# Kernel optimization log

Measured on AMD Instinct MI355X. Metric: run time of the kernel, lower is better.

Reference implementation:

```python
import jax, jax.numpy as jnp
import numpy as np

H, W = 512, 512          # pseudo_image_dims
C = 32                   # feat_channels == MHA embed_dim
NH, HD = 2, 16           # heads, head_dim
B, NL, NR = 2, 50000, 20000
EPS = 1e-5
SCALE = np.float32(1.0 / np.sqrt(HD))

# 3x3 neighbor shifts used by shift_bev_grids (INDEX_SHIFT in source)
INDEX_SHIFT = jnp.array([[0, 0], [-1, 0], [1, 0], [0, 1], [-1, 1], [1, 1], [0, -1], [-1, -1], [1, -1]], dtype=jnp.int32)
# 5x5 shifts used by new_gen_dy_coor (gen_index_shift(2))
SHIFT25 = jnp.array([[i, j] for i in range(-2, 3) for j in range(-2, 3)], dtype=jnp.int32)


def _unique_coords(key, n):
    perm = jax.random.permutation(key, H * W)[:n]
    return jnp.stack([perm // W, perm % W], axis=1).astype(jnp.int32)


def setup_inputs():
    key = jax.random.key(0)
    ks = jax.random.split(key, 8)
    inp = {
        "li_bev_feats": jax.random.normal(ks[0], (B, NL, C), jnp.float32),
        "li_bev_coors": jnp.stack([_unique_coords(jax.random.fold_in(ks[1], b), NL) for b in range(B)]),
        "ra_bev_feats": jax.random.normal(ks[2], (B, NR, C), jnp.float32),
        "ra_bev_coors": jnp.stack([_unique_coords(jax.random.fold_in(ks[3], b), NR) for b in range(B)]),
        "radar_bev_dy": jax.random.bernoulli(ks[4], 0.3, (B, NR)),
    }
    pk = jax.random.split(ks[5], 12)
    w = lambda k, o, i: 0.05 * jax.random.normal(k, (o, i), jnp.float32)
    z = lambda n: jnp.zeros((n,), jnp.float32)
    inp.update(
        ln_li_w=jnp.ones((C,), jnp.float32), ln_li_b=z(C),
        ln_ra_w=jnp.ones((C,), jnp.float32), ln_ra_b=z(C),
        q1_w=w(pk[0], C, C), q1_b=z(C), k1_w=w(pk[1], C, C), k1_b=z(C), v1_w=w(pk[2], C, C), v1_b=z(C),
        q2_w=w(pk[3], C, C), q2_b=z(C), k2_w=w(pk[4], C, C), k2_b=z(C), v2_w=w(pk[5], C, C), v2_b=z(C),
        pos_w=w(pk[6], C, 2), pos_b=z(C),
        a1_in_w=w(pk[7], 3 * C, C), a1_in_b=z(3 * C), a1_out_w=w(pk[8], C, C), a1_out_b=z(C),
        a2_in_w=w(pk[9], 3 * C, C), a2_in_b=z(3 * C), a2_out_w=w(pk[10], C, C), a2_out_b=z(C),
    )
    return inp


def _ln(x, w, b):
    mu = jnp.mean(x, -1, keepdims=True)
    var = jnp.mean(jnp.square(x - mu), -1, keepdims=True)
    return (x - mu) / jnp.sqrt(var + EPS) * w + b


def _grid_of(coors, n):
    # dense coord -> pillar-index lookup table, -1 for empty cells
    return jnp.full((H, W), -1, jnp.int32).at[coors[:, 0], coors[:, 1]].set(jnp.arange(n, dtype=jnp.int32))


def _gather_kv(coors, grid, k_map, v_map, pe9):
    # per pillar: look up the 3x3 shifted neighbors in the OTHER modality's grid
    sh = coors[:, None, :] + INDEX_SHIFT[None]                      # [N,9,2]
    inb = (sh[..., 0] >= 0) & (sh[..., 0] < H) & (sh[..., 1] >= 0) & (sh[..., 1] < W)
    idx = grid[jnp.clip(sh[..., 0], 0, H - 1), jnp.clip(sh[..., 1], 0, W - 1)]
    valid = (inb & (idx >= 0))[..., None]                           # [N,9,1]
    safe = jnp.clip(idx, 0, None)
    k = jnp.where(valid, k_map[safe], 0.0)                          # masked_fill(~cond, 0)
    v = jnp.where(valid, v_map[safe] + pe9[None], 0.0)              # pos-enc added before masking
    return k, v


def _mha(q, k, v, Wi, bi, Wo, bo):
    # torch MultiheadAttention (batch_first, eval -> no dropout); q [N,1,C], k/v [N,9,C]
    n = q.shape[0]
    qp = (q @ Wi[:C].T + bi[:C]).reshape(n, 1, NH, HD)
    kp = (k @ Wi[C:2 * C].T + bi[C:2 * C]).reshape(n, -1, NH, HD)
    vp = (v @ Wi[2 * C:].T + bi[2 * C:]).reshape(n, -1, NH, HD)
    s = jnp.einsum("nqhd,nkhd->nhqk", qp, kp) * SCALE
    a = jax.nn.softmax(s, axis=-1)
    o = jnp.einsum("nhqk,nkhd->nqhd", a, vp).reshape(n, C)
    return o @ Wo.T + bo


def _scatter(coors, feat):
    # PointPillarsScatter: place [N,C] features at their (x,y) cells of a [C,H,W] canvas
    return jnp.zeros((H, W, C), feat.dtype).at[coors[:, 0], coors[:, 1]].set(feat).transpose(2, 0, 1)


def _forward(li_bev_feats, li_bev_coors, ra_bev_feats, ra_bev_coors, radar_bev_dy,
             ln_li_w, ln_li_b, ln_ra_w, ln_ra_b,
             q1_w, q1_b, k1_w, k1_b, v1_w, v1_b,
             q2_w, q2_b, k2_w, k2_b, v2_w, v2_b,
             pos_w, pos_b,
             a1_in_w, a1_in_b, a1_out_w, a1_out_b,
             a2_in_w, a2_in_b, a2_out_w, a2_out_b):
    pe9 = INDEX_SHIFT.astype(jnp.float32) @ pos_w.T + pos_b        # [9,C] positional codes

    def per_sample(li_f, li_c, ra_f, ra_c, ra_dy):
        li_n = _ln(li_f, ln_li_w, ln_li_b)
        ra_n = _ln(ra_f, ln_ra_w, ln_ra_b)
        li_grid = _grid_of(li_c, NL)
        ra_grid = _grid_of(ra_c, NR)
        # new_gen_dy_coor: lidar pillars within a 5x5 (mod dims+1) window of any dynamic radar pillar
        g = jnp.array([H + 1, W + 1], jnp.int32)
        sh = (ra_c[:, None, :] + SHIFT25[None]) % g                # [NR,25,2]
        inb = (sh[..., 0] < H) & (sh[..., 1] < W)
        idx = li_grid[jnp.clip(sh[..., 0], 0, H - 1), jnp.clip(sh[..., 1], 0, W - 1)]
        valid = inb & (idx >= 0) & ra_dy[:, None]
        dy_mask = jnp.zeros(NL + 1, bool).at[jnp.where(valid, idx, NL).reshape(-1)].set(True)[:NL]
        # branch 1: dynamic lidar queries cross-attend to 3x3 radar neighbors
        q1 = li_n @ q1_w.T + q1_b
        k1 = ra_n @ k1_w.T + k1_b
        v1 = ra_n @ v1_w.T + v1_b
        k, v = _gather_kv(li_c, ra_grid, k1, v1, pe9)
        out1 = _mha(q1[:, None, :], k, v, a1_in_w, a1_in_b, a1_out_w, a1_out_b)
        out1 = out1 * dy_mask[:, None].astype(out1.dtype)          # only dy pillars scattered
        img_li = _scatter(li_c, out1)
        # branch 2: radar queries cross-attend to 3x3 lidar neighbors
        q2 = ra_n @ q2_w.T + q2_b
        k2 = li_n @ k2_w.T + k2_b
        v2 = li_n @ v2_w.T + v2_b
        k, v = _gather_kv(ra_c, li_grid, k2, v2, pe9)
        out2 = _mha(q2[:, None, :], k, v, a2_in_w, a2_in_b, a2_out_w, a2_out_b)
        img_ra = _scatter(ra_c, out2)
        return img_li, img_ra

    return jax.vmap(per_sample)(li_bev_feats, li_bev_coors, ra_bev_feats, ra_bev_coors, radar_bev_dy)


def reference(li_bev_feats, li_bev_coors, ra_bev_feats, ra_bev_coors, radar_bev_dy,
              ln_li_w, ln_li_b, ln_ra_w, ln_ra_b,
              q1_w, q1_b, k1_w, k1_b, v1_w, v1_b,
              q2_w, q2_b, k2_w, k2_b, v2_w, v2_b,
              pos_w, pos_b,
              a1_in_w, a1_in_b, a1_out_w, a1_out_b,
              a2_in_w, a2_in_b, a2_out_w, a2_out_b):
    return _forward(li_bev_feats, li_bev_coors, ra_bev_feats, ra_bev_coors, radar_bev_dy,
                    ln_li_w, ln_li_b, ln_ra_w, ln_ra_b,
                    q1_w, q1_b, k1_w, k1_b, v1_w, v1_b,
                    q2_w, q2_b, k2_w, k2_b, v2_w, v2_b,
                    pos_w, pos_b,
                    a1_in_w, a1_in_b, a1_out_w, a1_out_b,
                    a2_in_w, a2_in_b, a2_out_w, a2_out_b)
```

## Files before the change

### kernel.cpp

```cpp
#include <hip/hip_runtime.h>
#include <stdint.h>

constexpr int Hh = 512, Ww = 512;
constexpr int HW = Hh * Ww;
constexpr int C  = 32;
constexpr int B  = 2;
constexpr int NL = 50000;
constexpr int NR = 20000;
constexpr float EPS = 1e-5f;
constexpr float SCALE = 0.25f;

constexpr int GBL = (NL + NR + 255) / 256;
constexpr int LB  = (NL + 255) / 256;
constexpr int RB  = (NR + 255) / 256;
constexpr int NTILE = 1024;

__device__ __constant__ int DX9[9] = {0,-1,1,0,-1,1,0,-1,1};
__device__ __constant__ int DY9[9] = {0,0,0,1,1,1,-1,-1,-1};

__device__ __forceinline__ int xcd_swz(int bid, int nb) {
    int q = nb >> 3, r = nb & 7;
    int xcd = bid & 7, idx = bid >> 3;
    return (xcd < r) ? xcd * (q + 1) + idx : r * (q + 1) + (xcd - r) * q + idx;
}

__global__ void count_k(const int* __restrict__ li_c, const int* __restrict__ ra_c,
                        int* __restrict__ cnt) {
    int b = blockIdx.y;
    int i = blockIdx.x * 256 + threadIdx.x;
    if (i < NL) {
        int x = li_c[((size_t)b * NL + i) * 2 + 0];
        int y = li_c[((size_t)b * NL + i) * 2 + 1];
        int tile = ((x >> 4) << 5) | (y >> 4);
        atomicAdd(&cnt[(b * 2 + 0) * NTILE + tile], 1);
    } else if (i < NL + NR) {
        int j = i - NL;
        int x = ra_c[((size_t)b * NR + j) * 2 + 0];
        int y = ra_c[((size_t)b * NR + j) * 2 + 1];
        int tile = ((x >> 4) << 5) | (y >> 4);
        atomicAdd(&cnt[(b * 2 + 1) * NTILE + tile], 1);
    }
}

__global__ void scan_k(const int* __restrict__ cnt, int* __restrict__ cursor) {
    int g = blockIdx.x;
    const int* c = cnt + g * NTILE;
    int* cur = cursor + g * NTILE;
    __shared__ int s[NTILE];
    int t = threadIdx.x;
    int self = c[t];
    s[t] = self;
    __syncthreads();
    for (int off = 1; off < NTILE; off <<= 1) {
        int v = (t >= off) ? s[t - off] : 0;
        __syncthreads();
        s[t] += v;
        __syncthreads();
    }
    cur[t] = s[t] - self;
}

__global__ void scatter_proj_k(const int* __restrict__ li_c, const int* __restrict__ ra_c,
                               const int* __restrict__ ra_dy,
                               int* __restrict__ li_grid, int* __restrict__ ra_grid,
                               uint8_t* __restrict__ rdy_grid, int* __restrict__ cursor,
                               int* __restrict__ lixy, int* __restrict__ raxy,
                               const float* __restrict__ li_f, const float* __restrict__ ra_f,
                               const float* __restrict__ ln_li_w, const float* __restrict__ ln_li_b,
                               const float* __restrict__ ln_ra_w, const float* __restrict__ ln_ra_b,
                               const float* __restrict__ a1iw, const float* __restrict__ a1ib,
                               const float* __restrict__ a2iw, const float* __restrict__ a2ib,
                               const float* __restrict__ q1w, const float* __restrict__ q1b,
                               const float* __restrict__ k1w, const float* __restrict__ k1b,
                               const float* __restrict__ v1w, const float* __restrict__ v1b,
                               const float* __restrict__ q2w, const float* __restrict__ q2b,
                               const float* __restrict__ k2w, const float* __restrict__ k2b,
                               const float* __restrict__ v2w, const float* __restrict__ v2b,
                               float* __restrict__ qp1, float* __restrict__ kp1, float* __restrict__ vp1,
                               float* __restrict__ qp2, float* __restrict__ kp2, float* __restrict__ vp2) {
    int bx = blockIdx.x, b = blockIdx.y, t = threadIdx.x;
    bool lidar = (bx < LB);
    int n = lidar ? NL : NR;
    int i = (lidar ? bx : bx - LB) * 256 + t;

    const float* feats = lidar ? li_f : ra_f;
    const float* lnw = lidar ? ln_li_w : ln_ra_w;
    const float* lnb = lidar ? ln_li_b : ln_ra_b;
    const float* Asec[3] = { (lidar ? a1iw : a2iw) + 0 * C * C,
                             (lidar ? a2iw : a1iw) + 1 * C * C,
                             (lidar ? a2iw : a1iw) + 2 * C * C };
    const float* absec[3] = { (lidar ? a1ib : a2ib) + 0 * C,
                              (lidar ? a2ib : a1ib) + 1 * C,
                              (lidar ? a2ib : a1ib) + 2 * C };
    const float* Wsec[3] = { lidar ? q1w : q2w, lidar ? k2w : k1w, lidar ? v2w : v1w };
    const float* bsec[3] = { lidar ? q1b : q2b, lidar ? k2b : k1b, lidar ? v2b : v1b };
    float* outp[3] = { lidar ? qp1 : qp2, lidar ? kp2 : kp1, lidar ? vp2 : vp1 };

    __shared__ float sM[3][1024];
    __shared__ float sc[3][32];
    for (int p = t; p < 3072; p += 256) {
        int m = p >> 10, e = p & 1023, r = e >> 5, d = e & 31;
        float s = 0.f;
        #pragma unroll
        for (int c = 0; c < C; ++c) s += Asec[m][r * C + c] * Wsec[m][c * C + d];
        sM[m][e] = s;
    }
    if (t < 96) {
        int m = t >> 5, r = t & 31;
        float s = absec[m][r];
        #pragma unroll
        for (int c = 0; c < C; ++c) s += Asec[m][r * C + c] * bsec[m][c];
        sc[m][r] = s;
    }
    __syncthreads();
    if (i >= n) return;

    int x = (lidar ? li_c : ra_c)[((size_t)b * n + i) * 2 + 0];
    int y = (lidar ? li_c : ra_c)[((size_t)b * n + i) * 2 + 1];
    int tile = ((x >> 4) << 5) | (y >> 4);
    int mod = lidar ? 0 : 1;
    int slot = atomicAdd(&cursor[(b * 2 + mod) * NTILE + tile], 1);
    size_t cellg = (size_t)b * HW + x * Ww + y;
    if (lidar) {
        li_grid[cellg] = slot;
        lixy[(size_t)b * NL + slot] = (x << 16) | y;
    } else {
        ra_grid[cellg] = slot;
        raxy[(size_t)b * NR + slot] = (x << 16) | y;
        if (ra_dy[(size_t)b * n + i] != 0) rdy_grid[cellg] = 0;
    }

    float xv[C];
    const float4* f4 = (const float4*)(feats + ((size_t)b * n + i) * C);
    #pragma unroll
    for (int q = 0; q < 8; ++q) {
        float4 tv = f4[q];
        xv[4*q] = tv.x; xv[4*q+1] = tv.y; xv[4*q+2] = tv.z; xv[4*q+3] = tv.w;
    }
    float mu = 0.f;
    #pragma unroll
    for (int c = 0; c < C; ++c) mu += xv[c];
    mu *= (1.0f / C);
    float var = 0.f;
    #pragma unroll
    for (int c = 0; c < C; ++c) { float d = xv[c] - mu; var += d * d; }
    var *= (1.0f / C);
    float inv = 1.0f / sqrtf(var + EPS);
    #pragma unroll
    for (int c = 0; c < C; ++c) xv[c] = (xv[c] - mu) * inv * lnw[c] + lnb[c];

    #pragma unroll
    for (int m = 0; m < 3; ++m) {
        float4* o4 = (float4*)(outp[m] + ((size_t)b * n + slot) * C);
        #pragma unroll
        for (int rq = 0; rq < 8; ++rq) {
            float4 tv;
            float* tp = &tv.x;
            #pragma unroll
            for (int rr = 0; rr < 4; ++rr) {
                int r = rq * 4 + rr;
                float s = sc[m][r];
                #pragma unroll
                for (int d = 0; d < C; ++d) s += sM[m][r * C + d] * xv[d];
                tp[rr] = s;
            }
            o4[rq] = tv;
        }
    }
}

__device__ __forceinline__ void attn_cell(
        int x, int y,
        const float* __restrict__ qrow,
        const float* __restrict__ kmap, const float* __restrict__ vmap,
        const int* __restrict__ kv_grid,
        const float* sWo, const float* sbo, const float* spe,
        const float* skinv, const float* svinv,
        float* v) {
    int nidx[9];
    #pragma unroll
    for (int j = 0; j < 9; ++j) {
        int sx = x + DX9[j], sy = y + DY9[j];
        nidx[j] = (sx >= 0 && sx < Hh && sy >= 0 && sy < Ww) ? kv_grid[sx * Ww + sy] : -1;
    }
    float qp[C];
    const float4* qp4 = (const float4*)qrow;
    #pragma unroll
    for (int q = 0; q < 8; ++q) {
        float4 tv = qp4[q];
        qp[4*q] = tv.x; qp[4*q+1] = tv.y; qp[4*q+2] = tv.z; qp[4*q+3] = tv.w;
    }
    float sc0[9], sc1[9];
    #pragma unroll
    for (int j = 0; j < 9; ++j) {
        int idx = nidx[j];
        const float4* kp4 = (idx >= 0) ? (const float4*)(kmap + (size_t)idx * C)
                                       : (const float4*)skinv;
        float s0 = 0.f, s1 = 0.f;
        #pragma unroll
        for (int q = 0; q < 4; ++q) {
            float4 tv = kp4[q];
            s0 += qp[4*q] * tv.x + qp[4*q+1] * tv.y + qp[4*q+2] * tv.z + qp[4*q+3] * tv.w;
        }
        #pragma unroll
        for (int q = 4; q < 8; ++q) {
            float4 tv = kp4[q];
            s1 += qp[4*q] * tv.x + qp[4*q+1] * tv.y + qp[4*q+2] * tv.z + qp[4*q+3] * tv.w;
        }
        sc0[j] = s0 * SCALE; sc1[j] = s1 * SCALE;
    }
    float m0 = sc0[0], m1 = sc1[0];
    #pragma unroll
    for (int j = 1; j < 9; ++j) { m0 = fmaxf(m0, sc0[j]); m1 = fmaxf(m1, sc1[j]); }
    float sum0 = 0.f, sum1 = 0.f;
    #pragma unroll
    for (int j = 0; j < 9; ++j) {
        sc0[j] = expf(sc0[j] - m0); sum0 += sc0[j];
        sc1[j] = expf(sc1[j] - m1); sum1 += sc1[j];
    }
    float r0 = 1.0f / sum0, r1 = 1.0f / sum1;

    float o[C];
    #pragma unroll
    for (int c = 0; c < C; ++c) o[c] = 0.f;
    #pragma unroll
    for (int j = 0; j < 9; ++j) {
        float a0 = sc0[j] * r0, a1 = sc1[j] * r1;
        int idx = nidx[j];
        if (idx >= 0) {
            const float4* vp4 = (const float4*)(vmap + (size_t)idx * C);
            #pragma unroll
            for (int q = 0; q < 8; ++q) {
                float4 tv = vp4[q];
                float a = (q < 4) ? a0 : a1;
                o[4*q]   += a * (tv.x + spe[j * 32 + 4*q]);
                o[4*q+1] += a * (tv.y + spe[j * 32 + 4*q+1]);
                o[4*q+2] += a * (tv.z + spe[j * 32 + 4*q+2]);
                o[4*q+3] += a * (tv.w + spe[j * 32 + 4*q+3]);
            }
        } else {
            #pragma unroll
            for (int d = 0; d < 16; ++d) {
                o[d]      += a0 * svinv[d];
                o[16 + d] += a1 * svinv[16 + d];
            }
        }
    }
    #pragma unroll
    for (int r = 0; r < C; ++r) {
        float s = sbo[r];
        #pragma unroll
        for (int c = 0; c < C; ++c) s += sWo[r * C + c] * o[c];
        v[r] = s;
    }
}

__global__ void attn_slot_k(const int* __restrict__ li_grid, const int* __restrict__ ra_grid,
                            const uint8_t* __restrict__ rdy_grid,
                            const int* __restrict__ lixy, const int* __restrict__ raxy,
                            const float* __restrict__ qp1, const float* __restrict__ kp1,
                            const float* __restrict__ vp1, const float* __restrict__ qp2,
                            const float* __restrict__ kp2, const float* __restrict__ vp2,
                            const float* __restrict__ a1iw, const float* __restrict__ a1ib,
                            const float* __restrict__ a2iw, const float* __restrict__ a2ib,
                            const float* __restrict__ posw, const float* __restrict__ posb,
                            const float* __restrict__ a1ow, const float* __restrict__ a1ob,
                            const float* __restrict__ a2ow, const float* __restrict__ a2ob,
                            float* __restrict__ feat1, float* __restrict__ feat2) {
    int wg = xcd_swz(blockIdx.x, LB + RB);
    bool br1 = (wg < LB);
    int n = br1 ? NL : NR;
    int i = (br1 ? wg : wg - LB) * 256 + threadIdx.x;
    int b = blockIdx.y;
    int t = threadIdx.x;

    const float* Wo = br1 ? a1ow : a2ow;
    const float* bo = br1 ? a1ob : a2ob;
    const float* Aib = br1 ? a1ib : a2ib;
    const float* Av  = (br1 ? a1iw : a2iw) + 2 * C * C;
    __shared__ alignas(16) float sWo[1024];
    __shared__ alignas(16) float sbo[32], skinv[32], svinv[32];
    __shared__ alignas(16) float spe[288];
    for (int p = t; p < 1024; p += 256) sWo[p] = Wo[p];
    if (t < 32) {
        sbo[t] = bo[t];
        skinv[t] = Aib[32 + t];
        svinv[t] = Aib[64 + t];
    }
    for (int e = t; e < 288; e += 256) {
        int j = e >> 5, r = e & 31;
        float sx = (float)DX9[j], sy = (float)DY9[j];
        float s = 0.f;
        #pragma unroll
        for (int c = 0; c < C; ++c) {
            float pe = posw[c * 2 + 0] * sx + posw[c * 2 + 1] * sy + posb[c];
            s += Av[r * C + c] * pe;
        }
        spe[e] = s;
    }
    __syncthreads();
    if (i >= n) return;

    int pc = (br1 ? lixy : raxy)[(size_t)b * n + i];
    int x = pc >> 16, y = pc & 0xFFFF;

    float v[C];
    if (br1) {
        const uint8_t* rdy = rdy_grid + (size_t)b * HW;
        bool dy = false;
        #pragma unroll
        for (int dx = -2; dx <= 2 && !dy; ++dx) {
            int cx = x + dx;
            cx = (cx < 0) ? cx + 513 : (cx >= 513 ? cx - 513 : cx);
            if (cx == 512) continue;
            #pragma unroll
            for (int dyy = -2; dyy <= 2; ++dyy) {
                int cy = y + dyy;
                cy = (cy < 0) ? cy + 513 : (cy >= 513 ? cy - 513 : cy);
                if (cy == 512) continue;
                if (rdy[cx * Ww + cy] == 0) { dy = true; break; }
            }
        }
        if (dy) {
            attn_cell(x, y, qp1 + ((size_t)b * NL + i) * C,
                      kp1 + (size_t)b * NR * C, vp1 + (size_t)b * NR * C,
                      ra_grid + (size_t)b * HW, sWo, sbo, spe, skinv, svinv, v);
        } else {
            #pragma unroll
            for (int c = 0; c < C; ++c) v[c] = 0.f;
        }
        float4* o4 = (float4*)(feat1 + ((size_t)b * NL + i) * C);
        #pragma unroll
        for (int q = 0; q < 8; ++q) o4[q] = *(float4*)&v[4*q];
    } else {
        attn_cell(x, y, qp2 + ((size_t)b * NR + i) * C,
                  kp2 + (size_t)b * NL * C, vp2 + (size_t)b * NL * C,
                  li_grid + (size_t)b * HW, sWo, sbo, spe, skinv, svinv, v);
        float4* o4 = (float4*)(feat2 + ((size_t)b * NR + i) * C);
        #pragma unroll
        for (int q = 0; q < 8; ++q) o4[q] = *(float4*)&v[4*q];
    }
}

__global__ void canvas_k(const int* __restrict__ li_grid, const int* __restrict__ ra_grid,
                         const float* __restrict__ feat1, const float* __restrict__ feat2,
                         float* __restrict__ out_li, float* __restrict__ out_ra) {
    int b = blockIdx.y;
    int wg = xcd_swz(blockIdx.x, HW / 256);
    int cell = wg * 256 + threadIdx.x;
    size_t gidx = (size_t)b * HW + cell;
    size_t obase = (size_t)b * C * HW + cell;

    int li = li_grid[gidx];
    float v[C];
    if (li >= 0) {
        const float4* f = (const float4*)(feat1 + ((size_t)b * NL + li) * C);
        #pragma unroll
        for (int q = 0; q < 8; ++q) {
            float4 t = f[q];
            v[4*q] = t.x; v[4*q+1] = t.y; v[4*q+2] = t.z; v[4*q+3] = t.w;
        }
    } else {
        #pragma unroll
        for (int c = 0; c < C; ++c) v[c] = 0.f;
    }
    #pragma unroll
    for (int c = 0; c < C; ++c) out_li[obase + (size_t)c * HW] = v[c];

    int ra = ra_grid[gidx];
    if (ra >= 0) {
        const float4* f = (const float4*)(feat2 + ((size_t)b * NR + ra) * C);
        #pragma unroll
        for (int q = 0; q < 8; ++q) {
            float4 t = f[q];
            v[4*q] = t.x; v[4*q+1] = t.y; v[4*q+2] = t.z; v[4*q+3] = t.w;
        }
    } else {
        #pragma unroll
        for (int c = 0; c < C; ++c) v[c] = 0.f;
    }
    #pragma unroll
    for (int c = 0; c < C; ++c) out_ra[obase + (size_t)c * HW] = v[c];
}

extern "C" void kernel_launch(void* const* d_in, const int* in_sizes, int n_in,
                              void* d_out, int out_size, void* d_ws, size_t ws_size,
                              hipStream_t stream) {
    const float*   li_f  = (const float*)d_in[0];
    const int*     li_c  = (const int*)d_in[1];
    const float*   ra_f  = (const float*)d_in[2];
    const int*     ra_c  = (const int*)d_in[3];
    const int*     ra_dy = (const int*)d_in[4];
    const float* ln_li_w = (const float*)d_in[5];
    const float* ln_li_b = (const float*)d_in[6];
    const float* ln_ra_w = (const float*)d_in[7];
    const float* ln_ra_b = (const float*)d_in[8];
    const float* q1w = (const float*)d_in[9],  *q1b = (const float*)d_in[10];
    const float* k1w = (const float*)d_in[11], *k1b = (const float*)d_in[12];
    const float* v1w = (const float*)d_in[13], *v1b = (const float*)d_in[14];
    const float* q2w = (const float*)d_in[15], *q2b = (const float*)d_in[16];
    const float* k2w = (const float*)d_in[17], *k2b = (const float*)d_in[18];
    const float* v2w = (const float*)d_in[19], *v2b = (const float*)d_in[20];
    const float* posw = (const float*)d_in[21], *posb = (const float*)d_in[22];
    const float* a1iw = (const float*)d_in[23], *a1ib = (const float*)d_in[24];
    const float* a1ow = (const float*)d_in[25], *a1ob = (const float*)d_in[26];
    const float* a2iw = (const float*)d_in[27], *a2ib = (const float*)d_in[28];
    const float* a2ow = (const float*)d_in[29], *a2ob = (const float*)d_in[30];

    char* ws = (char*)d_ws;
    size_t off = 0;
    auto carve = [&](size_t bytes) { void* p = ws + off; off += (bytes + 255) & ~(size_t)255; return p; };
    int*     li_grid  = (int*)carve((size_t)B * HW * 4);
    int*     ra_grid  = (int*)carve((size_t)B * HW * 4);
    uint8_t* rdy_grid = (uint8_t*)carve((size_t)B * HW);
    size_t   init_bytes = off;
    int*     cnt      = (int*)carve((size_t)4 * NTILE * 4);
    int*     cursor   = (int*)carve((size_t)4 * NTILE * 4);
    int*     lixy     = (int*)carve((size_t)B * NL * 4);
    int*     raxy     = (int*)carve((size_t)B * NR * 4);
    float*   qp1 = (float*)carve((size_t)B * NL * C * 4);
    float*   kp1 = (float*)carve((size_t)B * NR * C * 4);
    float*   vp1 = (float*)carve((size_t)B * NR * C * 4);
    float*   qp2 = (float*)carve((size_t)B * NR * C * 4);
    float*   kp2 = (float*)carve((size_t)B * NL * C * 4);
    float*   vp2 = (float*)carve((size_t)B * NL * C * 4);
    float*   feat1 = (float*)carve((size_t)B * NL * C * 4);
    float*   feat2 = (float*)carve((size_t)B * NR * C * 4);
    (void)ws_size; (void)n_in; (void)in_sizes; (void)out_size;

    float* out_li = (float*)d_out;
    float* out_ra = out_li + (size_t)B * C * HW;

    hipMemsetAsync(li_grid, 0xFF, init_bytes, stream);
    hipMemsetAsync(cnt, 0, (size_t)4 * NTILE * 4, stream);

    count_k<<<dim3(GBL, B), dim3(256), 0, stream>>>(li_c, ra_c, cnt);
    scan_k<<<dim3(4), dim3(NTILE), 0, stream>>>(cnt, cursor);
    scatter_proj_k<<<dim3(LB + RB, B), dim3(256), 0, stream>>>(
        li_c, ra_c, ra_dy, li_grid, ra_grid, rdy_grid, cursor, lixy, raxy,
        li_f, ra_f, ln_li_w, ln_li_b, ln_ra_w, ln_ra_b,
        a1iw, a1ib, a2iw, a2ib,
        q1w, q1b, k1w, k1b, v1w, v1b, q2w, q2b, k2w, k2b, v2w, v2b,
        qp1, kp1, vp1, qp2, kp2, vp2);
    attn_slot_k<<<dim3(LB + RB, B), dim3(256), 0, stream>>>(
        li_grid, ra_grid, rdy_grid, lixy, raxy,
        qp1, kp1, vp1, qp2, kp2, vp2,
        a1iw, a1ib, a2iw, a2ib, posw, posb, a1ow, a1ob, a2ow, a2ob,
        feat1, feat2);
    canvas_k<<<dim3(HW / 256, B), dim3(256), 0, stream>>>(
        li_grid, ra_grid, feat1, feat2, out_li, out_ra);
}
```

Before: 405.3 us.

## Split attention across two threads per query, one per head, and drop XCD swizzle

The attention kernel now assigns two threads to each query, one per head. Each thread computes its head's scores, softmax and weighted V sum, plus a partial output projection, and the partials are combined with a lane shuffle. This cuts per-thread register pressure and doubles the thread count, aiming for better occupancy and latency hiding on the gathers. The XCD block swizzle is also removed from the attention and canvas kernels, which may change L2 locality. The cost is duplicated neighbor-index lookups and dynamic-check work in both threads.

```diff
diff --git a/kernel.cpp b/kernel.cpp
--- a/kernel.cpp
+++ b/kernel.cpp
@@ -13,16 +13,12 @@
 constexpr int GBL = (NL + NR + 255) / 256;
 constexpr int LB  = (NL + 255) / 256;
 constexpr int RB  = (NR + 255) / 256;
+constexpr int LB2 = (NL + 127) / 128;
+constexpr int RB2 = (NR + 127) / 128;
 constexpr int NTILE = 1024;
 
 __device__ __constant__ int DX9[9] = {0,-1,1,0,-1,1,0,-1,1};
 __device__ __constant__ int DY9[9] = {0,0,0,1,1,1,-1,-1,-1};
-
-__device__ __forceinline__ int xcd_swz(int bid, int nb) {
-    int q = nb >> 3, r = nb & 7;
-    int xcd = bid & 7, idx = bid >> 3;
-    return (xcd < r) ? xcd * (q + 1) + idx : r * (q + 1) + (xcd - r) * q + idx;
-}
 
 __global__ void count_k(const int* __restrict__ li_c, const int* __restrict__ ra_c,
                         int* __restrict__ cnt) {
@@ -169,92 +165,6 @@
     }
 }
 
-__device__ __forceinline__ void attn_cell(
-        int x, int y,
-        const float* __restrict__ qrow,
-        const float* __restrict__ kmap, const float* __restrict__ vmap,
-        const int* __restrict__ kv_grid,
-        const float* sWo, const float* sbo, const float* spe,
-        const float* skinv, const float* svinv,
-        float* v) {
-    int nidx[9];
-    #pragma unroll
-    for (int j = 0; j < 9; ++j) {
-        int sx = x + DX9[j], sy = y + DY9[j];
-        nidx[j] = (sx >= 0 && sx < Hh && sy >= 0 && sy < Ww) ? kv_grid[sx * Ww + sy] : -1;
-    }
-    float qp[C];
-    const float4* qp4 = (const float4*)qrow;
-    #pragma unroll
-    for (int q = 0; q < 8; ++q) {
-        float4 tv = qp4[q];
-        qp[4*q] = tv.x; qp[4*q+1] = tv.y; qp[4*q+2] = tv.z; qp[4*q+3] = tv.w;
-    }
-    float sc0[9], sc1[9];
-    #pragma unroll
-    for (int j = 0; j < 9; ++j) {
-        int idx = nidx[j];
-        const float4* kp4 = (idx >= 0) ? (const float4*)(kmap + (size_t)idx * C)
-                                       : (const float4*)skinv;
-        float s0 = 0.f, s1 = 0.f;
-        #pragma unroll
-        for (int q = 0; q < 4; ++q) {
-            float4 tv = kp4[q];
-            s0 += qp[4*q] * tv.x + qp[4*q+1] * tv.y + qp[4*q+2] * tv.z + qp[4*q+3] * tv.w;
-        }
-        #pragma unroll
-        for (int q = 4; q < 8; ++q) {
-            float4 tv = kp4[q];
-            s1 += qp[4*q] * tv.x + qp[4*q+1] * tv.y + qp[4*q+2] * tv.z + qp[4*q+3] * tv.w;
-        }
-        sc0[j] = s0 * SCALE; sc1[j] = s1 * SCALE;
-    }
-    float m0 = sc0[0], m1 = sc1[0];
-    #pragma unroll
-    for (int j = 1; j < 9; ++j) { m0 = fmaxf(m0, sc0[j]); m1 = fmaxf(m1, sc1[j]); }
-    float sum0 = 0.f, sum1 = 0.f;
-    #pragma unroll
-    for (int j = 0; j < 9; ++j) {
-        sc0[j] = expf(sc0[j] - m0); sum0 += sc0[j];
-        sc1[j] = expf(sc1[j] - m1); sum1 += sc1[j];
-    }
-    float r0 = 1.0f / sum0, r1 = 1.0f / sum1;
-
-    float o[C];
-    #pragma unroll
-    for (int c = 0; c < C; ++c) o[c] = 0.f;
-    #pragma unroll
-    for (int j = 0; j < 9; ++j) {
-        float a0 = sc0[j] * r0, a1 = sc1[j] * r1;
-        int idx = nidx[j];
-        if (idx >= 0) {
-            const float4* vp4 = (const float4*)(vmap + (size_t)idx * C);
-            #pragma unroll
-            for (int q = 0; q < 8; ++q) {
-                float4 tv = vp4[q];
-                float a = (q < 4) ? a0 : a1;
-                o[4*q]   += a * (tv.x + spe[j * 32 + 4*q]);
-                o[4*q+1] += a * (tv.y + spe[j * 32 + 4*q+1]);
-                o[4*q+2] += a * (tv.z + spe[j * 32 + 4*q+2]);
-                o[4*q+3] += a * (tv.w + spe[j * 32 + 4*q+3]);
-            }
-        } else {
-            #pragma unroll
-            for (int d = 0; d < 16; ++d) {
-                o[d]      += a0 * svinv[d];
-                o[16 + d] += a1 * svinv[16 + d];
-            }
-        }
-    }
-    #pragma unroll
-    for (int r = 0; r < C; ++r) {
-        float s = sbo[r];
-        #pragma unroll
-        for (int c = 0; c < C; ++c) s += sWo[r * C + c] * o[c];
-        v[r] = s;
-    }
-}
-
 __global__ void attn_slot_k(const int* __restrict__ li_grid, const int* __restrict__ ra_grid,
                             const uint8_t* __restrict__ rdy_grid,
                             const int* __restrict__ lixy, const int* __restrict__ raxy,
@@ -267,12 +177,13 @@
                             const float* __restrict__ a1ow, const float* __restrict__ a1ob,
                             const float* __restrict__ a2ow, const float* __restrict__ a2ob,
                             float* __restrict__ feat1, float* __restrict__ feat2) {
-    int wg = xcd_swz(blockIdx.x, LB + RB);
-    bool br1 = (wg < LB);
+    int bx = blockIdx.x;
+    bool br1 = (bx < LB2);
     int n = br1 ? NL : NR;
-    int i = (br1 ? wg : wg - LB) * 256 + threadIdx.x;
+    int t = threadIdx.x;
+    int qi = (br1 ? bx : bx - LB2) * 128 + (t >> 1);
+    int h  = t & 1;
     int b = blockIdx.y;
-    int t = threadIdx.x;
 
     const float* Wo = br1 ? a1ow : a2ow;
     const float* bo = br1 ? a1ob : a2ob;
@@ -299,12 +210,12 @@
         spe[e] = s;
     }
     __syncthreads();
-    if (i >= n) return;
-
-    int pc = (br1 ? lixy : raxy)[(size_t)b * n + i];
+    if (qi >= n) return;
+
+    int pc = (br1 ? lixy : raxy)[(size_t)b * n + qi];
     int x = pc >> 16, y = pc & 0xFFFF;
-
-    float v[C];
+    float* featrow = (br1 ? feat1 : feat2) + ((size_t)b * n + qi) * C;
+
     if (br1) {
         const uint8_t* rdy = rdy_grid + (size_t)b * HW;
         bool dy = false;
@@ -321,24 +232,105 @@
                 if (rdy[cx * Ww + cy] == 0) { dy = true; break; }
             }
         }
-        if (dy) {
-            attn_cell(x, y, qp1 + ((size_t)b * NL + i) * C,
-                      kp1 + (size_t)b * NR * C, vp1 + (size_t)b * NR * C,
-                      ra_grid + (size_t)b * HW, sWo, sbo, spe, skinv, svinv, v);
+        if (!dy) {
+            if (h == 0) {
+                float4 z = {0.f, 0.f, 0.f, 0.f};
+                float4* o4 = (float4*)featrow;
+                #pragma unroll
+                for (int q = 0; q < 8; ++q) o4[q] = z;
+            }
+            return;
+        }
+    }
+
+    const int* kv_grid = (br1 ? ra_grid : li_grid) + (size_t)b * HW;
+    int nkv = br1 ? NR : NL;
+    const float* kmap = (br1 ? kp1 : kp2) + (size_t)b * nkv * C;
+    const float* vmap = (br1 ? vp1 : vp2) + (size_t)b * nkv * C;
+
+    int nidx[9];
+    #pragma unroll
+    for (int j = 0; j < 9; ++j) {
+        int sx = x + DX9[j], sy = y + DY9[j];
+        nidx[j] = (sx >= 0 && sx < Hh && sy >= 0 && sy < Ww) ? kv_grid[sx * Ww + sy] : -1;
+    }
+
+    float qh[16];
+    {
+        const float4* q4 = (const float4*)((br1 ? qp1 : qp2) + ((size_t)b * n + qi) * C + h * 16);
+        #pragma unroll
+        for (int q = 0; q < 4; ++q) {
+            float4 tv = q4[q];
+            qh[4*q] = tv.x; qh[4*q+1] = tv.y; qh[4*q+2] = tv.z; qh[4*q+3] = tv.w;
+        }
+    }
+
+    float sc[9];
+    #pragma unroll
+    for (int j = 0; j < 9; ++j) {
+        int idx = nidx[j];
+        const float4* kp4 = (idx >= 0) ? (const float4*)(kmap + (size_t)idx * C + h * 16)
+                                       : (const float4*)(skinv + h * 16);
+        float s = 0.f;
+        #pragma unroll
+        for (int q = 0; q < 4; ++q) {
+            float4 tv = kp4[q];
+            s += qh[4*q] * tv.x + qh[4*q+1] * tv.y + qh[4*q+2] * tv.z + qh[4*q+3] * tv.w;
+        }
+        sc[j] = s * SCALE;
+    }
+    float m0 = sc[0];
+    #pragma unroll
+    for (int j = 1; j < 9; ++j) m0 = fmaxf(m0, sc[j]);
+    float sum = 0.f;
+    #pragma unroll
+    for (int j = 0; j < 9; ++j) { sc[j] = expf(sc[j] - m0); sum += sc[j]; }
+    float rs = 1.0f / sum;
+
+    float o[16];
+    #pragma unroll
+    for (int d = 0; d < 16; ++d) o[d] = 0.f;
+    #pragma unroll
+    for (int j = 0; j < 9; ++j) {
+        float a = sc[j] * rs;
+        int idx = nidx[j];
+        if (idx >= 0) {
+            const float4* vp4 = (const float4*)(vmap + (size_t)idx * C + h * 16);
+            #pragma unroll
+            for (int q = 0; q < 4; ++q) {
+                float4 tv = vp4[q];
+                o[4*q]   += a * (tv.x + spe[j * 32 + h * 16 + 4*q]);
+                o[4*q+1] += a * (tv.y + spe[j * 32 + h * 16 + 4*q+1]);
+                o[4*q+2] += a * (tv.z + spe[j * 32 + h * 16 + 4*q+2]);
+                o[4*q+3] += a * (tv.w + spe[j * 32 + h * 16 + 4*q+3]);
+            }
         } else {
             #pragma unroll
-            for (int c = 0; c < C; ++c) v[c] = 0.f;
-        }
-        float4* o4 = (float4*)(feat1 + ((size_t)b * NL + i) * C);
-        #pragma unroll
-        for (int q = 0; q < 8; ++q) o4[q] = *(float4*)&v[4*q];
-    } else {
-        attn_cell(x, y, qp2 + ((size_t)b * NR + i) * C,
-                  kp2 + (size_t)b * NL * C, vp2 + (size_t)b * NL * C,
-                  li_grid + (size_t)b * HW, sWo, sbo, spe, skinv, svinv, v);
-        float4* o4 = (float4*)(feat2 + ((size_t)b * NR + i) * C);
-        #pragma unroll
-        for (int q = 0; q < 8; ++q) o4[q] = *(float4*)&v[4*q];
+            for (int d = 0; d < 16; ++d) o[d] += a * svinv[h * 16 + d];
+        }
+    }
+
+    float P[32];
+    #pragma unroll
+    for (int r = 0; r < C; ++r) {
+        float s = 0.f;
+        #pragma unroll
+        for (int c = 0; c < 16; ++c) s += sWo[r * C + h * 16 + c] * o[c];
+        P[r] = s;
+    }
+    #pragma unroll
+    for (int r = 0; r < C; ++r) P[r] += __shfl_xor(P[r], 1);
+    if (h == 0) {
+        float4* o4 = (float4*)featrow;
+        #pragma unroll
+        for (int rq = 0; rq < 8; ++rq) {
+            float4 tv;
+            tv.x = P[4*rq]   + sbo[4*rq];
+            tv.y = P[4*rq+1] + sbo[4*rq+1];
+            tv.z = P[4*rq+2] + sbo[4*rq+2];
+            tv.w = P[4*rq+3] + sbo[4*rq+3];
+            o4[rq] = tv;
+        }
     }
 }
 
@@ -346,8 +338,7 @@
                          const float* __restrict__ feat1, const float* __restrict__ feat2,
                          float* __restrict__ out_li, float* __restrict__ out_ra) {
     int b = blockIdx.y;
-    int wg = xcd_swz(blockIdx.x, HW / 256);
-    int cell = wg * 256 + threadIdx.x;
+    int cell = blockIdx.x * 256 + threadIdx.x;
     size_t gidx = (size_t)b * HW + cell;
     size_t obase = (size_t)b * C * HW + cell;
 
@@ -442,7 +433,7 @@
         a1iw, a1ib, a2iw, a2ib,
         q1w, q1b, k1w, k1b, v1w, v1b, q2w, q2b, k2w, k2b, v2w, v2b,
         qp1, kp1, vp1, qp2, kp2, vp2);
-    attn_slot_k<<<dim3(LB + RB, B), dim3(256), 0, stream>>>(
+    attn_slot_k<<<dim3(LB2 + RB2, B), dim3(256), 0, stream>>>(
         li_grid, ra_grid, rdy_grid, lixy, raxy,
         qp1, kp1, vp1, qp2, kp2, vp2,
         a1iw, a1ib, a2iw, a2ib, posw, posb, a1ow, a1ob, a2ow, a2ob,
```

Result: faster. 348.3 us (-14.1%).
